# Performance work log

Measured on AMD Instinct MI355X. Metric: run time of the kernel, lower is better.

Reference implementation:

```python
import jax, jax.numpy as jnp
import numpy as np
import itertools, math

N_QUBITS = 16
HW_K = 8
N_LAYERS = 32
BATCH = 256
N_STATES = math.comb(N_QUBITS, HW_K)  # 12870


def _list_gates():
    gates = []
    for l in range(N_LAYERS):
        gates += [(q, q + 1) for q in range(l % 2, N_QUBITS - 1, 2)]
    return gates  # 240 gates


def _build_pairs(n, k, list_gates):
    # basis of Hamming-weight-k states, indexed as in map_RBS
    basis = list(itertools.combinations(range(n), k))
    idx = {s: i for i, s in enumerate(basis)}
    cache = {}
    rows = []
    for (i, j) in list_gates:
        if (i, j) not in cache:
            others = [q for q in range(n) if q != i and q != j]
            pr = []
            for s in itertools.combinations(others, k - 1):
                a = idx[tuple(sorted(s + (i,)))]
                b = idx[tuple(sorted(s + (j,)))]
                pr.append((a, b))
            cache[(i, j)] = pr
        rows.append(cache[(i, j)])
    return np.asarray(rows, dtype=np.int32)  # [G, P, 2], P = binom(n-2, k-1)


def setup_inputs() -> dict:
    key = jax.random.key(0)
    k1, k2 = jax.random.split(key)
    gates = _list_gates()
    pairs = jnp.asarray(_build_pairs(N_QUBITS, HW_K, gates))
    input_state = jax.random.normal(k1, (BATCH, N_STATES), dtype=jnp.float32)
    angles = jax.random.uniform(k2, (len(gates),), dtype=jnp.float32)  # nn.Parameter init torch.rand
    return {"input_state": input_state, "angles": angles, "pairs": pairs}


def reference(input_state, angles, pairs):
    # Each RBS gate applies, per affected pair (i, j) of basis states:
    #   y[i] =  cos(t) x[i] + sin(t) x[j]
    #   y[j] = -sin(t) x[i] + cos(t) x[j]
    # which is exactly (cos_matrix*cos + sin_matrix*sin + id_matrix) @ x.
    def step(state, gate):
        theta, pr = gate
        ii, jj = pr[:, 0], pr[:, 1]
        xi = state[:, ii]  # [B, P]
        xj = state[:, jj]
        c, s = jnp.cos(theta), jnp.sin(theta)
        state = state.at[:, ii].set(c * xi + s * xj)
        state = state.at[:, jj].set(c * xj - s * xi)
        return state, None

    out, _ = jax.lax.scan(step, input_state, (angles, pairs))
    return out
```

## Files before the change

### kernel.cpp

```cpp
#include <hip/hip_runtime.h>
#include <stdint.h>

#define NSTATES 12870
#define NPAD2   18376
#define NGATES  240
#define PERIOD  15
#define NLP     16
#define TPB     1024
#define NPAIRU  858

#define CS_OFF      0
#define P01_OFF     1920
#define P23_OFF     5352
#define BND_OFF     8784
#define M2_OFF      4032
#define M1_OFF      14112
#define PERM_OFF    31824
#define WS_NEED     57564
#define DYNLDS      (NPAD2 * 4)

__device__ __constant__ uint8_t FREEPOS[10] = {0,1,2,5,6,9,10,13,14,15};
__device__ __constant__ uint8_t IDPOS[16] = {0,1,2,3,4,5,6,7,8,9,10,11,12,13,14,15};
__device__ __constant__ uint8_t LRANK[16] = {0,0,1,0,2,1,2,0,3,3,4,1,5,2,3,0};
__device__ __constant__ uint8_t NBT[5]  = {1,4,6,4,1};
__device__ __constant__ uint8_t PPAD[5] = {1,5,7,5,1};
__device__ __constant__ uint8_t PAX2[5] = {1,5,7,5,1};
__device__ __constant__ uint8_t  CLSW0[21] = {0,4,0,4,0,4, 1,1,2,2,3,3, 1,1,1, 2,2,2, 3,3,3};
__device__ __constant__ uint8_t  CLSW1[21] = {1,1,2,2,3,3, 0,4,0,4,0,4, 1,2,3, 1,2,3, 1,2,3};
__device__ __constant__ uint16_t CLSS[22] =
  {0,8,64,92,120,176,184,192,248,276,304,360,368,396,452,522,578,648,704,774,830,858};

__global__ __launch_bounds__(256) void prep_fused(
    const float* __restrict__ angles, uint8_t* __restrict__ ws) {
  __shared__ int C[17][9];
  __shared__ int SECB[5][5][5];
  if (threadIdx.x == 0) {
    for (int n = 0; n <= 16; ++n)
      for (int k = 0; k <= 8; ++k)
        C[n][k] = (k == 0) ? 1 : ((k > n) ? 0 : C[n-1][k-1] + C[n-1][k]);
    int acc = 0;
    for (int a0 = 0; a0 < 5; ++a0)
      for (int a1 = 0; a1 < 5; ++a1)
        for (int a2 = 0; a2 < 5; ++a2) {
          SECB[a0][a1][a2] = acc;
          int a3 = 8 - a0 - a1 - a2;
          if (a3 >= 0 && a3 <= 4) acc += NBT[a0] * NBT[a1] * PAX2[a2] * PPAD[a3];
        }
  }
  __syncthreads();

  auto permof = [&](uint32_t mask) -> int {
    int g0 = mask & 15, g1 = (mask >> 4) & 15, g2 = (mask >> 8) & 15, g3 = (mask >> 12) & 15;
    int w0 = __popc(g0), w1 = __popc(g1), w2 = __popc(g2), w3 = __popc(g3);
    return SECB[w0][w1][w2] +
           ((LRANK[g0] * NBT[w1] + LRANK[g1]) * PAX2[w2] + LRANK[g2]) * PPAD[w3] + LRANK[g3];
  };
  auto unrank_mask = [&](int n, int k, int r, const uint8_t* pos) -> uint32_t {
    uint32_t m = 0; int v = 0;
    for (int i = 0; i < k; ++i) {
      for (;;) { int cnt = C[n - 1 - v][k - 1 - i]; if (r < cnt) break; r -= cnt; ++v; }
      m |= 1u << pos[v]; ++v;
    }
    return m;
  };

  int u = blockIdx.x * 256 + threadIdx.x;
  if (u < 2 * NPAIRU) {
    const bool is01 = (u < NPAIRU);
    const int uu = is01 ? u : u - NPAIRU;
    int c = 0;
    while (c < 20 && uu >= (int)CLSS[c + 1]) ++c;
    int r = uu - CLSS[c];
    const int wa = CLSW0[c], wb = CLSW1[c];
    const int W = 8 - wa - wb;
    int wc = 0, wd = 0, lc = 0, ld = 0;
    for (wc = 0; wc <= 4; ++wc) {
      wd = W - wc; if (wd < 0 || wd > 4) continue;
      int n = NBT[wc] * NBT[wd];
      if (r < n) { lc = r / NBT[wd]; ld = r % NBT[wd]; break; }
      r -= n;
    }
    if (is01) {
      int base = SECB[wa][wb][wc] + lc * PPAD[wd] + ld;
      int strd = PAX2[wc] * PPAD[wd];
      ((uint32_t*)(ws + P01_OFF))[uu] = (uint32_t)base | ((uint32_t)strd << 16);
    } else {
      int base = SECB[wc][wd][wa] + (lc * NBT[wd] + ld) * PAX2[wa] * PPAD[wb];
      int pstr = PPAD[wb];
      ((uint32_t*)(ws + P23_OFF))[uu] = (uint32_t)base | ((uint32_t)pstr << 16);
    }
  } else if (u < 2 * NPAIRU + 3744) {
    int v = u - 2 * NPAIRU;
    uint8_t* bnd = ws + BND_OFF;
    const uint32_t XL[3] = {1u << 3, 1u << 7, 1u << 11};
    const uint32_t XB[3] = {(1u<<3)|(1u<<4), (1u<<7)|(1u<<8), (1u<<11)|(1u<<12)};
    if (v < 252) {
      uint32_t mo = unrank_mask(10, 5, v, FREEPOS);
      uint32_t rep = mo | XL[0] | XL[1] | XL[2];
      uint32_t mm[8];
      for (int beta = 0; beta < 8; ++beta) {
        uint32_t m = rep;
        if (beta & 1) m ^= XB[0];
        if (beta & 2) m ^= XB[1];
        if (beta & 4) m ^= XB[2];
        mm[beta] = permof(m);
      }
      uint32_t* o = (uint32_t*)bnd + (size_t)v * 4;
      o[0] = mm[0] | (mm[1] << 16); o[1] = mm[2] | (mm[3] << 16);
      o[2] = mm[4] | (mm[5] << 16); o[3] = mm[6] | (mm[7] << 16);
    } else if (v < 1512) {
      int q = v - 252, cls = q / 420, o2 = q % 420;
      int gA = (cls == 2) ? 1 : 0;
      int gB = (cls == 0) ? 1 : 2;
      int gC = 3 - gA - gB;
      int vv = (o2 < 210) ? 0 : 1, oo = vv ? o2 - 210 : o2;
      uint32_t mo = unrank_mask(10, 6 - 2 * vv, oo, FREEPOS);
      uint32_t rep = mo | XL[gA] | XL[gB] | (vv ? XB[gC] : 0u);
      uint32_t mm[4];
      for (int beta = 0; beta < 4; ++beta) {
        uint32_t m = rep;
        if (beta & 1) m ^= XB[gA];
        if (beta & 2) m ^= XB[gB];
        mm[beta] = permof(m);
      }
      uint32_t* o = (uint32_t*)(bnd + M2_OFF + (size_t)cls * 3360) + (size_t)o2 * 2;
      o[0] = mm[0] | (mm[1] << 16); o[1] = mm[2] | (mm[3] << 16);
    } else {
      int q = v - 1512, cls = q / 744, o2 = q % 744;
      int ia = (cls == 0) ? 1 : 0;
      int ib = (cls == 2) ? 1 : 2;
      int v1, v2, f, oo;
      if      (o2 < 120) { v1 = 0; v2 = 0; f = 7; oo = o2; }
      else if (o2 < 372) { v1 = 0; v2 = 1; f = 5; oo = o2 - 120; }
      else if (o2 < 624) { v1 = 1; v2 = 0; f = 5; oo = o2 - 372; }
      else               { v1 = 1; v2 = 1; f = 3; oo = o2 - 624; }
      uint32_t mo = unrank_mask(10, f, oo, FREEPOS);
      uint32_t rep = mo | XL[cls] | (v1 ? XB[ia] : 0u) | (v2 ? XB[ib] : 0u);
      uint32_t m0 = permof(rep), m1 = permof(rep ^ XB[cls]);
      *((uint32_t*)(bnd + M1_OFF + (size_t)cls * 2976) + o2) = m0 | (m1 << 16);
    }
  } else if (u < 2 * NPAIRU + 3744 + NGATES) {
    int g = u - (2 * NPAIRU + 3744);
    float t = angles[g];
    ((float2*)(ws + CS_OFF))[g] = make_float2(cosf(t), sinf(t));
  } else if (u < 2 * NPAIRU + 3744 + NGATES + NSTATES) {
    int r = u - (2 * NPAIRU + 3744 + NGATES);
    uint32_t mask = unrank_mask(16, 8, r, IDPOS);
    ((uint16_t*)(ws + PERM_OFF))[r] = (uint16_t)permof(mask);
  }
}

__device__ __forceinline__ void rot(float& rx, float& ry, const float2 cs) {
  float nx = fmaf(cs.x, rx, cs.y * ry);
  float ny = fmaf(cs.x, ry, -cs.y * rx);
  rx = nx; ry = ny;
}
__device__ __forceinline__ float lds_ld(const float* st, uint32_t boff) {
  return *(const float*)((const char*)st + boff);
}
__device__ __forceinline__ void lds_st(float* st, uint32_t boff, float v) {
  *(float*)((char*)st + boff) = v;
}

template<int W, int S>
__device__ __forceinline__ void mix_axis(float* x, const float2 a1, const float2 a2, const float2 a3) {
  if constexpr (W == 1) {
    rot(x[0], x[S], a1); rot(x[2*S], x[3*S], a2); rot(x[S], x[2*S], a3);
  } else if constexpr (W == 2) {
    rot(x[S], x[2*S], a1);   rot(x[3*S], x[4*S], a1);
    rot(x[S], x[3*S], a2);   rot(x[2*S], x[4*S], a2);
    rot(x[0], x[S], a3);     rot(x[4*S], x[5*S], a3);
  } else if constexpr (W == 3) {
    rot(x[2*S], x[3*S], a1); rot(x[0], x[S], a2); rot(x[S], x[2*S], a3);
  }
}

template<int KA, int KB>
__device__ __forceinline__ void do_unit(float* st, uint32_t base, uint32_t sA, uint32_t sB,
    const float2 a1, const float2 a2, const float2 a3,
    const float2 b1, const float2 b2, const float2 b3) {
  constexpr int NA = (KA == 0) ? 1 : ((KA == 2) ? 6 : 4);
  constexpr int NB = (KB == 0) ? 1 : ((KB == 2) ? 6 : 4);
  float x[NA * NB];
#pragma unroll
  for (int ia = 0; ia < NA; ++ia)
#pragma unroll
    for (int ib = 0; ib < NB; ++ib)
      x[ia * NB + ib] = lds_ld(st, base + ia * sA + ib * sB);
  if constexpr (KA != 0) {
#pragma unroll
    for (int ib = 0; ib < NB; ++ib) mix_axis<KA, NB>(&x[ib], a1, a2, a3);
  }
  if constexpr (KB != 0) {
#pragma unroll
    for (int ia = 0; ia < NA; ++ia) mix_axis<KB, 1>(&x[ia * NB], b1, b2, b3);
  }
#pragma unroll
  for (int ia = 0; ia < NA; ++ia)
#pragma unroll
    for (int ib = 0; ib < NB; ++ib)
      lds_st(st, base + ia * sA + ib * sB, x[ia * NB + ib]);
}

template<int KA, int KB, bool LIN>
__device__ __forceinline__ void run_unit(float* st, uint32_t md,
    const float2 a1, const float2 a2, const float2 a3,
    const float2 b1, const float2 b2, const float2 b3) {
  constexpr int NB = (KB == 0) ? 1 : ((KB == 2) ? 6 : 4);
  const uint32_t base = (md & 0xffffu) << 2;
  uint32_t sA, sB;
  if constexpr (LIN) { sB = (md >> 16) << 2; sA = NB * sB; }
  else               { sA = (md >> 16) << 2; sB = 4; }
  do_unit<KA, KB>(st, base, sA, sB, a1, a2, a3, b1, b2, b3);
}

template<bool LIN>
__device__ __forceinline__ void dispatch_pair(int tid, float* st, uint32_t md,
    const float2 a1, const float2 a2, const float2 a3,
    const float2 b1, const float2 b2, const float2 b3) {
  if (tid < 368) {
    if (tid < 184) {
      if (tid < 64)       run_unit<0,1,LIN>(st, md, a1,a2,a3, b1,b2,b3);
      else if (tid < 120) run_unit<0,2,LIN>(st, md, a1,a2,a3, b1,b2,b3);
      else                run_unit<0,3,LIN>(st, md, a1,a2,a3, b1,b2,b3);
    } else {
      if (tid < 248)      run_unit<1,0,LIN>(st, md, a1,a2,a3, b1,b2,b3);
      else if (tid < 304) run_unit<2,0,LIN>(st, md, a1,a2,a3, b1,b2,b3);
      else                run_unit<3,0,LIN>(st, md, a1,a2,a3, b1,b2,b3);
    }
  } else {
    if (tid < 578) {
      if (tid < 396)      run_unit<1,1,LIN>(st, md, a1,a2,a3, b1,b2,b3);
      else if (tid < 452) run_unit<1,2,LIN>(st, md, a1,a2,a3, b1,b2,b3);
      else if (tid < 522) run_unit<1,3,LIN>(st, md, a1,a2,a3, b1,b2,b3);
      else                run_unit<2,1,LIN>(st, md, a1,a2,a3, b1,b2,b3);
    } else {
      if (tid < 648)      run_unit<2,2,LIN>(st, md, a1,a2,a3, b1,b2,b3);
      else if (tid < 704) run_unit<2,3,LIN>(st, md, a1,a2,a3, b1,b2,b3);
      else if (tid < 774) run_unit<3,1,LIN>(st, md, a1,a2,a3, b1,b2,b3);
      else if (tid < 830) run_unit<3,2,LIN>(st, md, a1,a2,a3, b1,b2,b3);
      else                run_unit<3,3,LIN>(st, md, a1,a2,a3, b1,b2,b3);
    }
  }
}

__global__ __launch_bounds__(TPB) void rbs_fused2(
    const float* __restrict__ in, const uint8_t* __restrict__ ws,
    float* __restrict__ out) {
  extern __shared__ float st[];
  __shared__ float2 csl[NGATES];
  const int tid = threadIdx.x;
  const size_t row = blockIdx.x;
  const uint16_t* __restrict__ perm16 = (const uint16_t*)(ws + PERM_OFF);

  { const float* src = in + row * NSTATES;
    for (int i = tid; i < NSTATES; i += TPB) st[perm16[i]] = src[i]; }
  if (tid < NGATES) csl[tid] = ((const float2*)(ws + CS_OFF))[tid];

  const uint32_t md01 = (tid < NPAIRU) ? ((const uint32_t*)(ws + P01_OFF))[tid] : 0u;
  const uint32_t md23 = (tid < NPAIRU) ? ((const uint32_t*)(ws + P23_OFF))[tid] : 0u;
  const uint8_t* bnd = ws + BND_OFF;
  uint4 bd[4];
#pragma unroll
  for (int k = 0; k < 4; ++k) {
    int u = tid + k * 1024;
    bd[k] = make_uint4(0u, 0u, 0u, 0u);
    if (u < 252) {
      bd[k] = ((const uint4*)bnd)[u];
    } else if (u < 1512) {
      int q = u - 252, cls = q / 420, o = q % 420;
      uint2 m = *(const uint2*)(bnd + M2_OFF + (size_t)cls * 3360 + (size_t)o * 8);
      bd[k].x = m.x; bd[k].y = m.y;
    } else if (u < 3744) {
      int q = u - 1512, cls = q / 744, o = q % 744;
      bd[k].x = *((const uint32_t*)(bnd + M1_OFF + (size_t)cls * 2976) + o);
    }
  }
  __syncthreads();

#pragma unroll 1
  for (int t = 0; t < NLP; ++t) {
    const int g0 = t * PERIOD;
    if (tid < NPAIRU)
      dispatch_pair<true>(tid, st, md01,
          csl[g0], csl[g0+1], csl[g0+8], csl[g0+2], csl[g0+3], csl[g0+10]);
    __syncthreads();
    if (tid < NPAIRU)
      dispatch_pair<false>(tid, st, md23,
          csl[g0+4], csl[g0+5], csl[g0+12], csl[g0+6], csl[g0+7], csl[g0+14]);
    __syncthreads();
    const float2 c0 = csl[g0 + 9], c1 = csl[g0 + 11], c2 = csl[g0 + 13];
#pragma unroll
    for (int k = 0; k < 4; ++k) {
      int u = tid + k * 1024;
      if (u >= 3744) break;
      uint4 d = bd[k];
      if (u < 252) {
        uint32_t e0 = (d.x & 0xffffu) << 2, e1 = (d.x >> 16) << 2;
        uint32_t e2 = (d.y & 0xffffu) << 2, e3 = (d.y >> 16) << 2;
        uint32_t e4 = (d.z & 0xffffu) << 2, e5 = (d.z >> 16) << 2;
        uint32_t e6 = (d.w & 0xffffu) << 2, e7 = (d.w >> 16) << 2;
        float x0 = lds_ld(st, e0), x1 = lds_ld(st, e1), x2 = lds_ld(st, e2), x3 = lds_ld(st, e3);
        float x4 = lds_ld(st, e4), x5 = lds_ld(st, e5), x6 = lds_ld(st, e6), x7 = lds_ld(st, e7);
        rot(x0, x1, c0); rot(x2, x3, c0); rot(x4, x5, c0); rot(x6, x7, c0);
        rot(x0, x2, c1); rot(x1, x3, c1); rot(x4, x6, c1); rot(x5, x7, c1);
        rot(x0, x4, c2); rot(x1, x5, c2); rot(x2, x6, c2); rot(x3, x7, c2);
        lds_st(st, e0, x0); lds_st(st, e1, x1); lds_st(st, e2, x2); lds_st(st, e3, x3);
        lds_st(st, e4, x4); lds_st(st, e5, x5); lds_st(st, e6, x6); lds_st(st, e7, x7);
      } else if (u < 1512) {
        int cls = (u - 252) / 420;
        float2 cA = (cls == 2) ? c1 : c0;
        float2 cB = (cls == 0) ? c1 : c2;
        uint32_t e0 = (d.x & 0xffffu) << 2, e1 = (d.x >> 16) << 2;
        uint32_t e2 = (d.y & 0xffffu) << 2, e3 = (d.y >> 16) << 2;
        float x0 = lds_ld(st, e0), x1 = lds_ld(st, e1), x2 = lds_ld(st, e2), x3 = lds_ld(st, e3);
        rot(x0, x1, cA); rot(x2, x3, cA);
        rot(x0, x2, cB); rot(x1, x3, cB);
        lds_st(st, e0, x0); lds_st(st, e1, x1); lds_st(st, e2, x2); lds_st(st, e3, x3);
      } else {
        int cls = (u - 1512) / 744;
        float2 cg = (cls == 0) ? c0 : ((cls == 1) ? c1 : c2);
        uint32_t e0 = (d.x & 0xffffu) << 2, e1 = (d.x >> 16) << 2;
        float x0 = lds_ld(st, e0), x1 = lds_ld(st, e1);
        rot(x0, x1, cg);
        lds_st(st, e0, x0); lds_st(st, e1, x1);
      }
    }
    __syncthreads();
  }

  { float* dst = out + row * NSTATES;
    for (int i = tid; i < NSTATES; i += TPB) dst[i] = st[perm16[i]]; }
}

__global__ __launch_bounds__(TPB) void rbs_raw(
    const float* __restrict__ in, const int* __restrict__ pairs_raw,
    const float* __restrict__ angles, float* __restrict__ out) {
  __shared__ float stx[NSTATES];
  __shared__ float2 csl[NGATES];
  const int tid = threadIdx.x;
  const size_t row = blockIdx.x;
  const float* src = in + row * NSTATES;
  for (int i = tid; i < NSTATES; i += TPB) stx[i] = src[i];
  for (int i = tid; i < NGATES; i += TPB) {
    float t = angles[i];
    csl[i] = make_float2(cosf(t), sinf(t));
  }
  __syncthreads();
  for (int g = 0; g < NGATES; ++g) {
    const float c = csl[g].x, s = csl[g].y;
    for (int p = tid; p < 3432; p += TPB) {
      int2 ab = ((const int2*)pairs_raw)[(size_t)g * 3432 + p];
      float xi = stx[ab.x], xj = stx[ab.y];
      stx[ab.x] = fmaf(c, xi, s * xj);
      stx[ab.y] = fmaf(c, xj, -s * xi);
    }
    __syncthreads();
  }
  float* dst = out + row * NSTATES;
  for (int i = tid; i < NSTATES; i += TPB) dst[i] = stx[i];
}

extern "C" void kernel_launch(void* const* d_in, const int* in_sizes, int n_in,
                              void* d_out, int out_size, void* d_ws, size_t ws_size,
                              hipStream_t stream) {
  const float* in = (const float*)d_in[0];
  const float* angles = (const float*)d_in[1];
  const int* pairs = (const int*)d_in[2];
  float* out = (float*)d_out;

  if (d_ws != nullptr && ws_size >= WS_NEED) {
    uint8_t* ws = (uint8_t*)d_ws;
    (void)hipFuncSetAttribute((const void*)rbs_fused2,
                              hipFuncAttributeMaxDynamicSharedMemorySize, DYNLDS);
    const int total = 2 * NPAIRU + 3744 + NGATES + NSTATES;
    prep_fused<<<(total + 255) / 256, 256, 0, stream>>>(angles, ws);
    rbs_fused2<<<256, TPB, DYNLDS, stream>>>(in, ws, out);
  } else {
    rbs_raw<<<256, TPB, 0, stream>>>(in, pairs, angles, out);
  }
}
```

Before: 110.9 us.

## Realign pair-unit thread assignment to wavefront boundaries to reduce divergence

Remaps the 858 pair-block work units onto 1024 thread slots so that each 64-lane wavefront runs at most one or two unit template variants, splitting oversized classes across segments and padding gaps. The prep kernel now fills descriptor tables indexed by slot through segment lookup tables, and the main loop drops the tid<NPAIRU guard. mix_axis is also inlined into explicit rotations. The goal is to cut divergent serialization of different unrolled unit bodies within a wavefront, at the cost of some idle lanes and a larger workspace.

```diff
diff --git a/kernel.cpp b/kernel.cpp
--- a/kernel.cpp
+++ b/kernel.cpp
@@ -7,16 +7,15 @@
 #define PERIOD  15
 #define NLP     16
 #define TPB     1024
-#define NPAIRU  858
 
 #define CS_OFF      0
 #define P01_OFF     1920
-#define P23_OFF     5352
-#define BND_OFF     8784
+#define P23_OFF     6016
+#define BND_OFF     10112
 #define M2_OFF      4032
 #define M1_OFF      14112
-#define PERM_OFF    31824
-#define WS_NEED     57564
+#define PERM_OFF    33152
+#define WS_NEED     58892
 #define DYNLDS      (NPAD2 * 4)
 
 __device__ __constant__ uint8_t FREEPOS[10] = {0,1,2,5,6,9,10,13,14,15};
@@ -29,6 +28,11 @@
 __device__ __constant__ uint8_t  CLSW1[21] = {1,1,2,2,3,3, 0,4,0,4,0,4, 1,2,3, 1,2,3, 1,2,3};
 __device__ __constant__ uint16_t CLSS[22] =
   {0,8,64,92,120,176,184,192,248,276,304,360,368,396,452,522,578,648,704,774,830,858};
+__device__ __constant__ uint16_t SEG_S[18] = {0,64,128,192,256,320,384,412,448,512,576,640,704,768,832,896,902,908};
+__device__ __constant__ uint16_t SEG_E[18] = {64,120,192,256,312,384,412,440,504,576,632,704,760,832,888,902,908,914};
+__device__ __constant__ uint8_t  SEG_CA[18] = {0,2,4,6,8,10,12,20,13,14,15,16,17,18,19,14,16,18};
+__device__ __constant__ uint8_t  SEG_CB[18] = {1,3,5,7,9,11,255,255,255,255,255,255,255,255,255,255,255,255};
+__device__ __constant__ uint8_t  SEG_OF[18] = {0,0,0,0,0,0,0,0,0,0,0,0,0,0,0,64,64,64};
 
 __global__ __launch_bounds__(256) void prep_fused(
     const float* __restrict__ angles, uint8_t* __restrict__ ws) {
@@ -65,32 +69,38 @@
   };
 
   int u = blockIdx.x * 256 + threadIdx.x;
-  if (u < 2 * NPAIRU) {
-    const bool is01 = (u < NPAIRU);
-    const int uu = is01 ? u : u - NPAIRU;
-    int c = 0;
-    while (c < 20 && uu >= (int)CLSS[c + 1]) ++c;
-    int r = uu - CLSS[c];
-    const int wa = CLSW0[c], wb = CLSW1[c];
-    const int W = 8 - wa - wb;
-    int wc = 0, wd = 0, lc = 0, ld = 0;
-    for (wc = 0; wc <= 4; ++wc) {
-      wd = W - wc; if (wd < 0 || wd > 4) continue;
-      int n = NBT[wc] * NBT[wd];
-      if (r < n) { lc = r / NBT[wd]; ld = r % NBT[wd]; break; }
-      r -= n;
-    }
-    if (is01) {
-      int base = SECB[wa][wb][wc] + lc * PPAD[wd] + ld;
-      int strd = PAX2[wc] * PPAD[wd];
-      ((uint32_t*)(ws + P01_OFF))[uu] = (uint32_t)base | ((uint32_t)strd << 16);
-    } else {
-      int base = SECB[wc][wd][wa] + (lc * NBT[wd] + ld) * PAX2[wa] * PPAD[wb];
-      int pstr = PPAD[wb];
-      ((uint32_t*)(ws + P23_OFF))[uu] = (uint32_t)base | ((uint32_t)pstr << 16);
-    }
-  } else if (u < 2 * NPAIRU + 3744) {
-    int v = u - 2 * NPAIRU;
+  if (u < 2048) {
+    const bool is01 = (u < 1024);
+    const int slot = u & 1023;
+    int seg = -1;
+    for (int s2 = 0; s2 < 18; ++s2)
+      if (slot >= SEG_S[s2] && slot < SEG_E[s2]) { seg = s2; break; }
+    if (seg >= 0) {
+      int r = SEG_OF[seg] + (slot - SEG_S[seg]);
+      int c = SEG_CA[seg];
+      int sza = CLSS[c + 1] - CLSS[c];
+      if (SEG_CB[seg] != 255 && r >= sza) { r -= sza; c = SEG_CB[seg]; }
+      const int wa = CLSW0[c], wb = CLSW1[c];
+      const int W = 8 - wa - wb;
+      int wc, wd = 0, lc = 0, ld = 0;
+      for (wc = 0; wc <= 4; ++wc) {
+        wd = W - wc; if (wd < 0 || wd > 4) continue;
+        int n = NBT[wc] * NBT[wd];
+        if (r < n) { lc = r / NBT[wd]; ld = r % NBT[wd]; break; }
+        r -= n;
+      }
+      if (is01) {
+        int base = SECB[wa][wb][wc] + lc * PPAD[wd] + ld;
+        int strd = PAX2[wc] * PPAD[wd];
+        ((uint32_t*)(ws + P01_OFF))[slot] = (uint32_t)base | ((uint32_t)strd << 16);
+      } else {
+        int base = SECB[wc][wd][wa] + (lc * NBT[wd] + ld) * PAX2[wa] * PPAD[wb];
+        int pstr = PPAD[wb];
+        ((uint32_t*)(ws + P23_OFF))[slot] = (uint32_t)base | ((uint32_t)pstr << 16);
+      }
+    }
+  } else if (u < 2048 + 3744) {
+    int v = u - 2048;
     uint8_t* bnd = ws + BND_OFF;
     const uint32_t XL[3] = {1u << 3, 1u << 7, 1u << 11};
     const uint32_t XB[3] = {(1u<<3)|(1u<<4), (1u<<7)|(1u<<8), (1u<<11)|(1u<<12)};
@@ -139,12 +149,12 @@
       uint32_t m0 = permof(rep), m1 = permof(rep ^ XB[cls]);
       *((uint32_t*)(bnd + M1_OFF + (size_t)cls * 2976) + o2) = m0 | (m1 << 16);
     }
-  } else if (u < 2 * NPAIRU + 3744 + NGATES) {
-    int g = u - (2 * NPAIRU + 3744);
+  } else if (u < 2048 + 3744 + NGATES) {
+    int g = u - (2048 + 3744);
     float t = angles[g];
     ((float2*)(ws + CS_OFF))[g] = make_float2(cosf(t), sinf(t));
-  } else if (u < 2 * NPAIRU + 3744 + NGATES + NSTATES) {
-    int r = u - (2 * NPAIRU + 3744 + NGATES);
+  } else if (u < 2048 + 3744 + NGATES + NSTATES) {
+    int r = u - (2048 + 3744 + NGATES);
     uint32_t mask = unrank_mask(16, 8, r, IDPOS);
     ((uint16_t*)(ws + PERM_OFF))[r] = (uint16_t)permof(mask);
   }
@@ -160,19 +170,6 @@
 }
 __device__ __forceinline__ void lds_st(float* st, uint32_t boff, float v) {
   *(float*)((char*)st + boff) = v;
-}
-
-template<int W, int S>
-__device__ __forceinline__ void mix_axis(float* x, const float2 a1, const float2 a2, const float2 a3) {
-  if constexpr (W == 1) {
-    rot(x[0], x[S], a1); rot(x[2*S], x[3*S], a2); rot(x[S], x[2*S], a3);
-  } else if constexpr (W == 2) {
-    rot(x[S], x[2*S], a1);   rot(x[3*S], x[4*S], a1);
-    rot(x[S], x[3*S], a2);   rot(x[2*S], x[4*S], a2);
-    rot(x[0], x[S], a3);     rot(x[4*S], x[5*S], a3);
-  } else if constexpr (W == 3) {
-    rot(x[2*S], x[3*S], a1); rot(x[0], x[S], a2); rot(x[S], x[2*S], a3);
-  }
 }
 
 template<int KA, int KB>
@@ -187,13 +184,45 @@
 #pragma unroll
     for (int ib = 0; ib < NB; ++ib)
       x[ia * NB + ib] = lds_ld(st, base + ia * sA + ib * sB);
-  if constexpr (KA != 0) {
-#pragma unroll
-    for (int ib = 0; ib < NB; ++ib) mix_axis<KA, NB>(&x[ib], a1, a2, a3);
-  }
-  if constexpr (KB != 0) {
-#pragma unroll
-    for (int ia = 0; ia < NA; ++ia) mix_axis<KB, 1>(&x[ia * NB], b1, b2, b3);
+  if constexpr (KA == 1) {
+#pragma unroll
+    for (int ib = 0; ib < NB; ++ib) {
+      rot(x[0*NB+ib], x[1*NB+ib], a1); rot(x[2*NB+ib], x[3*NB+ib], a2);
+      rot(x[1*NB+ib], x[2*NB+ib], a3);
+    }
+  } else if constexpr (KA == 2) {
+#pragma unroll
+    for (int ib = 0; ib < NB; ++ib) {
+      rot(x[1*NB+ib], x[2*NB+ib], a1); rot(x[3*NB+ib], x[4*NB+ib], a1);
+      rot(x[1*NB+ib], x[3*NB+ib], a2); rot(x[2*NB+ib], x[4*NB+ib], a2);
+      rot(x[0*NB+ib], x[1*NB+ib], a3); rot(x[4*NB+ib], x[5*NB+ib], a3);
+    }
+  } else if constexpr (KA == 3) {
+#pragma unroll
+    for (int ib = 0; ib < NB; ++ib) {
+      rot(x[2*NB+ib], x[3*NB+ib], a1); rot(x[0*NB+ib], x[1*NB+ib], a2);
+      rot(x[1*NB+ib], x[2*NB+ib], a3);
+    }
+  }
+  if constexpr (KB == 1) {
+#pragma unroll
+    for (int ia = 0; ia < NA; ++ia) {
+      rot(x[ia*NB+0], x[ia*NB+1], b1); rot(x[ia*NB+2], x[ia*NB+3], b2);
+      rot(x[ia*NB+1], x[ia*NB+2], b3);
+    }
+  } else if constexpr (KB == 2) {
+#pragma unroll
+    for (int ia = 0; ia < NA; ++ia) {
+      rot(x[ia*NB+1], x[ia*NB+2], b1); rot(x[ia*NB+3], x[ia*NB+4], b1);
+      rot(x[ia*NB+1], x[ia*NB+3], b2); rot(x[ia*NB+2], x[ia*NB+4], b2);
+      rot(x[ia*NB+0], x[ia*NB+1], b3); rot(x[ia*NB+4], x[ia*NB+5], b3);
+    }
+  } else if constexpr (KB == 3) {
+#pragma unroll
+    for (int ia = 0; ia < NA; ++ia) {
+      rot(x[ia*NB+2], x[ia*NB+3], b1); rot(x[ia*NB+0], x[ia*NB+1], b2);
+      rot(x[ia*NB+1], x[ia*NB+2], b3);
+    }
   }
 #pragma unroll
   for (int ia = 0; ia < NA; ++ia)
@@ -218,29 +247,36 @@
 __device__ __forceinline__ void dispatch_pair(int tid, float* st, uint32_t md,
     const float2 a1, const float2 a2, const float2 a3,
     const float2 b1, const float2 b2, const float2 b3) {
-  if (tid < 368) {
-    if (tid < 184) {
-      if (tid < 64)       run_unit<0,1,LIN>(st, md, a1,a2,a3, b1,b2,b3);
-      else if (tid < 120) run_unit<0,2,LIN>(st, md, a1,a2,a3, b1,b2,b3);
-      else                run_unit<0,3,LIN>(st, md, a1,a2,a3, b1,b2,b3);
+  if (tid < 384) {
+    if (tid < 128) {
+      if (tid < 64)            run_unit<0,1,LIN>(st, md, a1,a2,a3, b1,b2,b3);
+      else if (tid < 120)      run_unit<0,2,LIN>(st, md, a1,a2,a3, b1,b2,b3);
+    } else if (tid < 256) {
+      if (tid < 192)           run_unit<0,3,LIN>(st, md, a1,a2,a3, b1,b2,b3);
+      else                     run_unit<1,0,LIN>(st, md, a1,a2,a3, b1,b2,b3);
     } else {
-      if (tid < 248)      run_unit<1,0,LIN>(st, md, a1,a2,a3, b1,b2,b3);
-      else if (tid < 304) run_unit<2,0,LIN>(st, md, a1,a2,a3, b1,b2,b3);
-      else                run_unit<3,0,LIN>(st, md, a1,a2,a3, b1,b2,b3);
-    }
-  } else {
-    if (tid < 578) {
-      if (tid < 396)      run_unit<1,1,LIN>(st, md, a1,a2,a3, b1,b2,b3);
-      else if (tid < 452) run_unit<1,2,LIN>(st, md, a1,a2,a3, b1,b2,b3);
-      else if (tid < 522) run_unit<1,3,LIN>(st, md, a1,a2,a3, b1,b2,b3);
-      else                run_unit<2,1,LIN>(st, md, a1,a2,a3, b1,b2,b3);
+      if (tid < 312)           run_unit<2,0,LIN>(st, md, a1,a2,a3, b1,b2,b3);
+      else if (tid >= 320)     run_unit<3,0,LIN>(st, md, a1,a2,a3, b1,b2,b3);
+    }
+  } else if (tid < 896) {
+    if (tid < 512) {
+      if (tid < 412)           run_unit<1,1,LIN>(st, md, a1,a2,a3, b1,b2,b3);
+      else if (tid < 440)      run_unit<3,3,LIN>(st, md, a1,a2,a3, b1,b2,b3);
+      else if (tid >= 448 && tid < 504) run_unit<1,2,LIN>(st, md, a1,a2,a3, b1,b2,b3);
+    } else if (tid < 640) {
+      if (tid < 576)           run_unit<1,3,LIN>(st, md, a1,a2,a3, b1,b2,b3);
+      else if (tid < 632)      run_unit<2,1,LIN>(st, md, a1,a2,a3, b1,b2,b3);
+    } else if (tid < 768) {
+      if (tid < 704)           run_unit<2,2,LIN>(st, md, a1,a2,a3, b1,b2,b3);
+      else if (tid < 760)      run_unit<2,3,LIN>(st, md, a1,a2,a3, b1,b2,b3);
     } else {
-      if (tid < 648)      run_unit<2,2,LIN>(st, md, a1,a2,a3, b1,b2,b3);
-      else if (tid < 704) run_unit<2,3,LIN>(st, md, a1,a2,a3, b1,b2,b3);
-      else if (tid < 774) run_unit<3,1,LIN>(st, md, a1,a2,a3, b1,b2,b3);
-      else if (tid < 830) run_unit<3,2,LIN>(st, md, a1,a2,a3, b1,b2,b3);
-      else                run_unit<3,3,LIN>(st, md, a1,a2,a3, b1,b2,b3);
-    }
+      if (tid < 832)           run_unit<3,1,LIN>(st, md, a1,a2,a3, b1,b2,b3);
+      else if (tid < 888)      run_unit<3,2,LIN>(st, md, a1,a2,a3, b1,b2,b3);
+    }
+  } else if (tid < 914) {
+    if (tid < 902)             run_unit<1,3,LIN>(st, md, a1,a2,a3, b1,b2,b3);
+    else if (tid < 908)        run_unit<2,2,LIN>(st, md, a1,a2,a3, b1,b2,b3);
+    else                       run_unit<3,1,LIN>(st, md, a1,a2,a3, b1,b2,b3);
   }
 }
 
@@ -257,8 +293,8 @@
     for (int i = tid; i < NSTATES; i += TPB) st[perm16[i]] = src[i]; }
   if (tid < NGATES) csl[tid] = ((const float2*)(ws + CS_OFF))[tid];
 
-  const uint32_t md01 = (tid < NPAIRU) ? ((const uint32_t*)(ws + P01_OFF))[tid] : 0u;
-  const uint32_t md23 = (tid < NPAIRU) ? ((const uint32_t*)(ws + P23_OFF))[tid] : 0u;
+  const uint32_t md01 = ((const uint32_t*)(ws + P01_OFF))[tid];
+  const uint32_t md23 = ((const uint32_t*)(ws + P23_OFF))[tid];
   const uint8_t* bnd = ws + BND_OFF;
   uint4 bd[4];
 #pragma unroll
@@ -281,13 +317,11 @@
 #pragma unroll 1
   for (int t = 0; t < NLP; ++t) {
     const int g0 = t * PERIOD;
-    if (tid < NPAIRU)
-      dispatch_pair<true>(tid, st, md01,
-          csl[g0], csl[g0+1], csl[g0+8], csl[g0+2], csl[g0+3], csl[g0+10]);
+    dispatch_pair<true>(tid, st, md01,
+        csl[g0], csl[g0+1], csl[g0+8], csl[g0+2], csl[g0+3], csl[g0+10]);
     __syncthreads();
-    if (tid < NPAIRU)
-      dispatch_pair<false>(tid, st, md23,
-          csl[g0+4], csl[g0+5], csl[g0+12], csl[g0+6], csl[g0+7], csl[g0+14]);
+    dispatch_pair<false>(tid, st, md23,
+        csl[g0+4], csl[g0+5], csl[g0+12], csl[g0+6], csl[g0+7], csl[g0+14]);
     __syncthreads();
     const float2 c0 = csl[g0 + 9], c1 = csl[g0 + 11], c2 = csl[g0 + 13];
 #pragma unroll
@@ -373,7 +407,7 @@
     uint8_t* ws = (uint8_t*)d_ws;
     (void)hipFuncSetAttribute((const void*)rbs_fused2,
                               hipFuncAttributeMaxDynamicSharedMemorySize, DYNLDS);
-    const int total = 2 * NPAIRU + 3744 + NGATES + NSTATES;
+    const int total = 2048 + 3744 + NGATES + NSTATES;
     prep_fused<<<(total + 255) / 256, 256, 0, stream>>>(angles, ws);
     rbs_fused2<<<256, TPB, DYNLDS, stream>>>(in, ws, out);
   } else {
```

Measured after the change: 122.0 us. 1.1x slower.
